# Optimization experiments

Measured on AMD Instinct MI355X. Metric: run time of the kernel, lower is better.

## Reference

```python
import jax, jax.numpy as jnp
import numpy as np

# NF4 codebook (bitsandbytes nf4 data type, 16 levels)
NF4_TABLE = np.array([
    -1.0, -0.6961928009986877, -0.5250730514526367, -0.39491748809814453,
    -0.28444138169288635, -0.18477343022823334, -0.09105003625154495, 0.0,
    0.07958029955625534, 0.16093020141124725, 0.24611230194568634,
    0.33791524171829224, 0.44070982933044434, 0.5626170039176941,
    0.7229568362236023, 1.0], dtype=np.float32)

BLOCKSIZE = 64
SCALING = 32.0 / 16.0  # lora_alpha / r


def setup_inputs() -> dict:
    key = jax.random.key(0)
    k1, k2, k3, k4, k5 = jax.random.split(key, 5)
    tokens, in_f, out_f, r = 256, 4096, 11008, 16
    x = jax.random.normal(k1, (tokens, in_f), dtype=jnp.float32)
    q_codes = jax.random.randint(k2, (out_f, in_f), 0, 16, dtype=jnp.int32)
    absmax = jax.random.uniform(k3, (out_f, in_f // BLOCKSIZE), dtype=jnp.float32)
    lora_A = jax.random.normal(k4, (r, in_f), dtype=jnp.float32) * (1.0 / np.sqrt(in_f))
    lora_B = jax.random.normal(k5, (out_f, r), dtype=jnp.float32) * 0.02
    return {"x": x, "q_codes": q_codes, "absmax": absmax,
            "lora_A": lora_A, "lora_B": lora_B}


def reference(x, q_codes, absmax, lora_A, lora_B):
    out_f, in_f = q_codes.shape
    nf4 = jnp.asarray(NF4_TABLE, dtype=x.dtype)
    # Dequantize: codebook lookup, then per-block absmax scale.
    W = nf4[q_codes].reshape(out_f, in_f // BLOCKSIZE, BLOCKSIZE)
    W = (W * absmax[:, :, None]).reshape(out_f, in_f)  # [out_f, in_f]
    # Base 4-bit linear (no bias in bnb Linear4bit default here).
    base = x @ W.T  # [tokens, out_f]
    # LoRA path: dropout p=0 is identity in eval; scaling = alpha/r.
    lora = (x @ lora_A.T) @ lora_B.T  # [tokens, r] -> [tokens, out_f]
    return base + lora * jnp.asarray(SCALING, dtype=x.dtype)
```

## Files before the change

kernel.cpp:

```cpp
#include <hip/hip_runtime.h>
#include <hip/hip_fp16.h>

typedef unsigned int uint;
typedef unsigned short ushort;

typedef __attribute__((ext_vector_type(8))) _Float16 f16x8;
typedef __attribute__((ext_vector_type(4))) float f32x4;

#define TOK 256
#define OUTF 11008
#define INF 4096
#define BM 256
#define BN 64
#define NT2 172

__device__ __constant__ float NF4_TBL[16] = {
    -1.0f, -0.6961928009986877f, -0.5250730514526367f, -0.39491748809814453f,
    -0.28444138169288635f, -0.18477343022823334f, -0.09105003625154495f, 0.0f,
    0.07958029955625534f, 0.16093020141124725f, 0.24611230194568634f,
    0.33791524171829224f, 0.44070982933044434f, 0.5626170039176941f,
    0.7229568362236023f, 1.0f};

__device__ __forceinline__ ushort f2h(float f) {
  return __half_as_ushort(__float2half(f));
}

__device__ __forceinline__ void async_cp16(const void* g, void* l) {
  __builtin_amdgcn_global_load_lds(
      (const __attribute__((address_space(1))) uint*)g,
      (__attribute__((address_space(3))) uint*)l, 16, 0, 0);
}

__device__ __forceinline__ float nf4v(int c, int tbits) {
  return __int_as_float(__builtin_amdgcn_ds_bpermute(c << 2, tbits));
}

__device__ __forceinline__ uint2 dq4(int4 c, __half2 ax2, int tbits) {
  __half2 h0 = __floats2half2_rn(nf4v(c.x, tbits), nf4v(c.y, tbits));
  __half2 h1 = __floats2half2_rn(nf4v(c.z, tbits), nf4v(c.w, tbits));
  h0 = __hmul2(h0, ax2);
  h1 = __hmul2(h1, ax2);
  union { __half2 h[2]; uint2 u; } r;
  r.h[0] = h0; r.h[1] = h1;
  return r.u;
}

__device__ __forceinline__ void step_barrier() {
  asm volatile("s_waitcnt lgkmcnt(0)" ::: "memory");
  __builtin_amdgcn_s_barrier();
}

__global__ void prep_kernel(const float* __restrict__ x, uint4* __restrict__ xf4,
                            const float4* __restrict__ lB4, ushort4* __restrict__ lBh4) {
  const int stride = gridDim.x * blockDim.x;
  const int t0 = blockIdx.x * blockDim.x + threadIdx.x;
  for (int f = t0; f < TOK * INF / 8; f += stride) {
    int l = f & 63;
    int rlo = l & 15, chunk = l >> 4;
    int ms = (f >> 6) & 7;
    int mt = ms >> 1, ks2 = ms & 1;
    int w = (f >> 9) & 3;
    int kb = f >> 11;
    int m = w * 64 + mt * 16 + rlo;
    int k0 = kb * 64 + (ks2 * 4 + chunk) * 8;
    const float4* src = (const float4*)(x + (size_t)m * INF + k0);
    float4 v0 = src[0], v1 = src[1];
    union { ushort4 h[2]; uint4 u; } pk;
    pk.h[0].x = f2h(v0.x); pk.h[0].y = f2h(v0.y); pk.h[0].z = f2h(v0.z); pk.h[0].w = f2h(v0.w);
    pk.h[1].x = f2h(v1.x); pk.h[1].y = f2h(v1.y); pk.h[1].z = f2h(v1.z); pk.h[1].w = f2h(v1.w);
    xf4[f] = pk.u;
  }
  for (int i = t0; i < OUTF * 16; i += stride) {
    int n = i >> 4, jq = i & 15;
    ushort4 o = {0, 0, 0, 0};
    if (jq < 4) {
      float4 v = lB4[n * 4 + jq];
      o.x = f2h(v.x); o.y = f2h(v.y); o.z = f2h(v.z); o.w = f2h(v.w);
    }
    lBh4[i] = o;
  }
}

__global__ __launch_bounds__(1024)
void xa_kernel(const float* __restrict__ x, const float* __restrict__ lA,
               ushort* __restrict__ xa2) {
  const int m = blockIdx.x;
  const int t = threadIdx.x;
  const float4* x4 = (const float4*)(x + (size_t)m * INF);
  const float4* lA4 = (const float4*)lA;
  float4 xv = x4[t];
  float acc[16];
#pragma unroll
  for (int j = 0; j < 16; ++j) {
    float4 a = lA4[j * (INF / 4) + t];
    acc[j] = xv.x * a.x + xv.y * a.y + xv.z * a.z + xv.w * a.w;
  }
#pragma unroll
  for (int j = 0; j < 16; ++j)
#pragma unroll
    for (int s = 32; s > 0; s >>= 1) acc[j] += __shfl_xor(acc[j], s, 64);
  __shared__ float red[16][16];
  const int w = t >> 6, l = t & 63;
  if (l == 0) {
#pragma unroll
    for (int j = 0; j < 16; ++j) red[w][j] = acc[j];
  }
  __syncthreads();
  if (t < 64) {
    ushort v = 0;
    if (t < 16) {
      float s = 0.f;
#pragma unroll
      for (int w2 = 0; w2 < 16; ++w2) s += red[w2][t];
      v = f2h(2.0f * s);
    }
    xa2[m * 64 + t] = v;
  }
}

__global__ __launch_bounds__(256, 2)
void gemm_kernel(const int* __restrict__ qc, const float* __restrict__ am,
                 const ushort* __restrict__ xf, const ushort* __restrict__ lBh,
                 const ushort* __restrict__ xa2, float* __restrict__ dest, int nst) {
  __shared__ ushort Bbuf[2][64 * 64];
  __shared__ float Qax[4096];

  const int tid = threadIdx.x;
  const int w = tid >> 6;
  const int l = tid & 63;
  const int chunk = l >> 4;
  const int rlo = l & 15;
  const int split = blockIdx.x / NT2;
  const int ntile = blockIdx.x - split * NT2;
  const int n0 = ntile * BN;
  const int kb0 = split * nst;

  const int tbits = __float_as_int(NF4_TBL[l & 15]);

  const int qrg = tid >> 4;
  const int qch = tid & 15;
  const int* qbase[4];
  int bdst[4];
#pragma unroll
  for (int p = 0; p < 4; ++p) {
    int r = p * 16 + qrg;
    qbase[p] = qc + (size_t)(n0 + r) * INF + kb0 * 64 + qch * 4;
    bdst[p] = r * 64 + (((qch >> 1) ^ (r & 7)) << 3) + (qch & 1) * 4;
  }

  int boff[2][4];
#pragma unroll
  for (int ks2 = 0; ks2 < 2; ++ks2)
#pragma unroll
    for (int nt = 0; nt < 4; ++nt)
      boff[ks2][nt] = (nt * 16 + rlo) * 64 + (((ks2 * 4 + chunk) ^ (rlo & 7)) << 3);

  f32x4 acc[4][4];
#pragma unroll
  for (int mt = 0; mt < 4; ++mt)
#pragma unroll
    for (int nt = 0; nt < 4; ++nt) acc[mt][nt] = (f32x4){0.f, 0.f, 0.f, 0.f};

  auto loadA = [&](f16x8 ar[2][4], int kb) {
    const ushort* base = xf + ((size_t)kb * 4 + w) * 4096 + (size_t)l * 8;
#pragma unroll
    for (int mt = 0; mt < 4; ++mt)
#pragma unroll
      for (int ks2 = 0; ks2 < 2; ++ks2)
        ar[ks2][mt] = *(const f16x8*)(base + (mt * 2 + ks2) * 512);
  };

  auto loadQ = [&](int4 q[4], int s) {
#pragma unroll
    for (int p = 0; p < 4; ++p) q[p] = *(const int4*)(qbase[p] + (size_t)s * 64);
  };

  auto dequantF = [&](int4 q[4], int kbt, ushort* bb) {
#pragma unroll
    for (int p = 0; p < 4; ++p) {
      int r = p * 16 + qrg;
      __half2 ax2 = __float2half2_rn(Qax[(kbt >> 2) * 256 + r * 4 + (kbt & 3)]);
      *(uint2*)&bb[bdst[p]] = dq4(q[p], ax2, tbits);
    }
  };

  auto compute = [&](f16x8 ar[2][4], const ushort* bb) {
    __builtin_amdgcn_s_setprio(1);
#pragma unroll
    for (int ks2 = 0; ks2 < 2; ++ks2) {
      f16x8 b[4];
#pragma unroll
      for (int nt = 0; nt < 4; ++nt) b[nt] = *(const f16x8*)&bb[boff[ks2][nt]];
#pragma unroll
      for (int mt = 0; mt < 4; ++mt)
#pragma unroll
        for (int nt = 0; nt < 4; ++nt)
          acc[mt][nt] = __builtin_amdgcn_mfma_f32_16x16x32_f16(ar[ks2][mt], b[nt], acc[mt][nt], 0, 0, 0);
    }
    __builtin_amdgcn_s_setprio(0);
  };

  if (w == 0) {
#pragma unroll
    for (int j = 0; j < 16; ++j)
      async_cp16(am + (size_t)(n0 + l) * 64 + j * 4, (char*)Qax + j * 1024);
  }
  f16x8 arA[2][4], arB[2][4];
  int4 qA[4], qB[4];
  loadA(arA, kb0);
  loadA(arB, kb0 + 1);
  loadQ(qA, 0);
  loadQ(qB, 1);
  __syncthreads();
  dequantF(qA, kb0, Bbuf[0]);
  step_barrier();

  for (int s = 0; s < nst; s += 2) {
    compute(arA, Bbuf[0]);
    if (s + 1 < nst) dequantF(qB, kb0 + s + 1, Bbuf[1]);
    if (s + 2 < nst) {
      loadA(arA, kb0 + s + 2);
      loadQ(qA, s + 2);
    }
    step_barrier();
    compute(arB, Bbuf[1]);
    if (s + 2 < nst) dequantF(qA, kb0 + s + 2, Bbuf[0]);
    if (s + 3 < nst) {
      loadA(arB, kb0 + s + 3);
      loadQ(qB, s + 3);
    }
    step_barrier();
  }

  if (split == 0) {
    f16x8 a_l[4], b_l[4];
#pragma unroll
    for (int mt = 0; mt < 4; ++mt)
      a_l[mt] = *(const f16x8*)(xa2 + (size_t)(w * 64 + mt * 16 + rlo) * 64 + chunk * 8);
#pragma unroll
    for (int nt = 0; nt < 4; ++nt)
      b_l[nt] = *(const f16x8*)(lBh + (size_t)(n0 + nt * 16 + rlo) * 64 + chunk * 8);
#pragma unroll
    for (int mt = 0; mt < 4; ++mt)
#pragma unroll
      for (int nt = 0; nt < 4; ++nt)
        acc[mt][nt] = __builtin_amdgcn_mfma_f32_16x16x32_f16(a_l[mt], b_l[nt], acc[mt][nt], 0, 0, 0);
  }

  float* dst = dest + (size_t)split * TOK * OUTF;
#pragma unroll
  for (int mt = 0; mt < 4; ++mt) {
#pragma unroll
    for (int nt = 0; nt < 4; ++nt) {
      int c = n0 + nt * 16 + rlo;
#pragma unroll
      for (int r = 0; r < 4; ++r) {
        int row = w * 64 + mt * 16 + chunk * 4 + r;
        dst[(size_t)row * OUTF + c] = acc[mt][nt][r];
      }
    }
  }
}

__global__ void reduce_kernel(const float4* __restrict__ part, float4* __restrict__ out,
                              int ks) {
  const int QN = TOK * OUTF / 4;
  int i = blockIdx.x * blockDim.x + threadIdx.x;
  if (i < QN) {
    float4 s = part[i];
    for (int s2 = 1; s2 < ks; ++s2) {
      float4 p = part[(size_t)s2 * QN + i];
      s.x += p.x; s.y += p.y; s.z += p.z; s.w += p.w;
    }
    out[i] = s;
  }
}

extern "C" void kernel_launch(void* const* d_in, const int* in_sizes, int n_in,
                              void* d_out, int out_size, void* d_ws, size_t ws_size,
                              hipStream_t stream) {
  const float* x = (const float*)d_in[0];
  const int* qc = (const int*)d_in[1];
  const float* am = (const float*)d_in[2];
  const float* lA = (const float*)d_in[3];
  const float* lB = (const float*)d_in[4];
  float* out = (float*)d_out;

  const size_t off_lB = (size_t)TOK * INF * 2;
  const size_t off_xa2 = off_lB + (size_t)OUTF * 64 * 2;
  const size_t off_part = off_xa2 + (size_t)TOK * 64 * 2;
  const size_t part_bytes = (size_t)TOK * OUTF * 4;

  ushort* xf = (ushort*)d_ws;
  ushort* lBh = (ushort*)((char*)d_ws + off_lB);
  ushort* xa2 = (ushort*)((char*)d_ws + off_xa2);
  float* part = (float*)((char*)d_ws + off_part);

  int ks = 1;
  if (ws_size >= off_part + 4 * part_bytes) ks = 4;
  else if (ws_size >= off_part + 2 * part_bytes) ks = 2;
  float* dest = (ks == 1) ? out : part;

  prep_kernel<<<2048, 256, 0, stream>>>(x, (uint4*)xf, (const float4*)lB,
                                        (ushort4*)lBh);
  xa_kernel<<<TOK, 1024, 0, stream>>>(x, lA, xa2);
  gemm_kernel<<<NT2 * ks, 256, 0, stream>>>(qc, am, xf, lBh, xa2, dest, 64 / ks);
  if (ks > 1)
    reduce_kernel<<<(TOK * OUTF / 4 + 255) / 256, 256, 0, stream>>>((const float4*)part,
                                                                    (float4*)out, ks);
}
```

Baseline: 318.2 us.

## Deepen quantized-weight prefetch to four stages in main K loop

Uses four register buffers for the packed NF4 weight codes instead of two, so each code load is issued four steps before it is dequantized. The loop is unrolled by four, and each step issues the next code prefetch before the MFMA compute, then loads the next A fragment and dequantizes the next tile. The goal is to hide global memory latency of the weight stream behind more compute. In exchange it adds 32 more VGPRs of in-flight data, which can raise register pressure and lower occupancy. It also relies on nst being a multiple of four, or on the guards handling the tail correctly.

```diff
diff --git a/kernel.cpp b/kernel.cpp
--- a/kernel.cpp
+++ b/kernel.cpp
@@ -206,31 +206,33 @@
       async_cp16(am + (size_t)(n0 + l) * 64 + j * 4, (char*)Qax + j * 1024);
   }
   f16x8 arA[2][4], arB[2][4];
-  int4 qA[4], qB[4];
+  int4 Q0[4], Q1[4], Q2[4], Q3[4];
   loadA(arA, kb0);
   loadA(arB, kb0 + 1);
-  loadQ(qA, 0);
-  loadQ(qB, 1);
+  loadQ(Q0, 0);
+  loadQ(Q1, 1);
+  loadQ(Q2, 2);
+  loadQ(Q3, 3);
   __syncthreads();
-  dequantF(qA, kb0, Bbuf[0]);
+  dequantF(Q0, kb0, Bbuf[0]);
   step_barrier();
 
-  for (int s = 0; s < nst; s += 2) {
-    compute(arA, Bbuf[0]);
-    if (s + 1 < nst) dequantF(qB, kb0 + s + 1, Bbuf[1]);
-    if (s + 2 < nst) {
-      loadA(arA, kb0 + s + 2);
-      loadQ(qA, s + 2);
-    }
-    step_barrier();
-    compute(arB, Bbuf[1]);
-    if (s + 2 < nst) dequantF(qA, kb0 + s + 2, Bbuf[0]);
-    if (s + 3 < nst) {
-      loadA(arB, kb0 + s + 3);
-      loadQ(qB, s + 3);
-    }
-    step_barrier();
-  }
+#define PIPE_STEP(s, AR, QDQ, QLD, BC, BN_)                    \
+  do {                                                         \
+    if ((s) + 4 < nst) loadQ(QLD, (s) + 4);                    \
+    compute(AR, Bbuf[BC]);                                     \
+    if ((s) + 2 < nst) loadA(AR, kb0 + (s) + 2);               \
+    if ((s) + 1 < nst) dequantF(QDQ, kb0 + (s) + 1, Bbuf[BN_]); \
+    step_barrier();                                            \
+  } while (0)
+
+  for (int s = 0; s < nst; s += 4) {
+    PIPE_STEP(s + 0, arA, Q1, Q0, 0, 1);
+    PIPE_STEP(s + 1, arB, Q2, Q1, 1, 0);
+    PIPE_STEP(s + 2, arA, Q3, Q2, 0, 1);
+    PIPE_STEP(s + 3, arB, Q0, Q3, 1, 0);
+  }
+#undef PIPE_STEP
 
   if (split == 0) {
     f16x8 a_l[4], b_l[4];
```

Measured after the change: 322.4 us. No clear change (+1.3%).
